# Performance work log

Measured on AMD Instinct MI355X. Metric: run time of the kernel, lower is better.

Reference implementation:

```python
import jax, jax.numpy as jnp
import numpy as np

B, T, I, H = 256, 512, 64, 128


def setup_inputs() -> dict:
    key = jax.random.key(0)
    ks = jax.random.split(key, 7)
    s_ih = 1.0 / np.sqrt(H)
    return {
        "inputs": jax.random.normal(ks[0], (B, T, I), dtype=jnp.float32),
        "h_prev": jax.random.normal(ks[1], (B, H), dtype=jnp.float32),
        "c_prev": jax.random.normal(ks[2], (B, H), dtype=jnp.float32),
        "W_ih": jax.random.uniform(ks[3], (4 * H, I), dtype=jnp.float32, minval=-s_ih, maxval=s_ih),
        "W_hh": jax.random.uniform(ks[4], (4 * H, H), dtype=jnp.float32, minval=-s_ih, maxval=s_ih),
        "b_ih": jax.random.uniform(ks[5], (4 * H,), dtype=jnp.float32, minval=-s_ih, maxval=s_ih),
        "b_hh": jax.random.uniform(ks[6], (4 * H,), dtype=jnp.float32, minval=-s_ih, maxval=s_ih),
    }


def reference(inputs, h_prev, c_prev, W_ih, W_hh, b_ih, b_hh):
    # Precompute input-to-gate projections for all timesteps in one GEMM: [B,T,4H]
    x_gates = jnp.einsum("bti,gi->btg", inputs, W_ih) + b_ih + b_hh

    def step(carry, xg):
        h, c = carry
        gates = xg + h @ W_hh.T  # [B, 4H]
        i_g, f_g, g_g, o_g = jnp.split(gates, 4, axis=-1)  # PyTorch i,f,g,o order
        i_g = jax.nn.sigmoid(i_g)
        f_g = jax.nn.sigmoid(f_g)
        g_g = jnp.tanh(g_g)
        o_g = jax.nn.sigmoid(o_g)
        c_next = f_g * c + i_g * g_g
        h_next = o_g * jnp.tanh(c_next)
        return (h_next, c_next), h_next

    (h_last, c_last), hs = jax.lax.scan(step, (h_prev, c_prev), jnp.swapaxes(x_gates, 0, 1))
    outputs = jnp.swapaxes(hs, 0, 1)  # [B, T, H]
    return outputs, h_last, c_last
```

## Files before the change

### kernel.cpp

```cpp
#include <hip/hip_runtime.h>


#define BB 256
#define TT 512
#define II 64
#define HH 128
#define KK 192
#define KS 8
#define KPT (KK / KS)
#define NTH (HH * KS)

static_assert(KPT % 4 == 0, "float4 granularity");

__device__ __forceinline__ float dpp_xor1(float v) {
    return __int_as_float(__builtin_amdgcn_mov_dpp(__float_as_int(v), 0xB1, 0xF, 0xF, true));
}
__device__ __forceinline__ float dpp_xor2(float v) {
    return __int_as_float(__builtin_amdgcn_mov_dpp(__float_as_int(v), 0x4E, 0xF, 0xF, true));
}
__device__ __forceinline__ float swz_xor4(float v) {
    return __int_as_float(__builtin_amdgcn_ds_swizzle(__float_as_int(v), 0x101F));
}
__device__ __forceinline__ float fast_sigmoid(float x) {
    float e = __expf(-x);
    return __builtin_amdgcn_rcpf(1.0f + e);
}
__device__ __forceinline__ float fast_tanh(float x) {
    float e = __expf(2.0f * x);
    return 1.0f - 2.0f * __builtin_amdgcn_rcpf(e + 1.0f);
}

__global__ __launch_bounds__(NTH, 4)
void lstm_split(const float* __restrict__ inputs,
                const float* __restrict__ h_prev,
                const float* __restrict__ c_prev,
                const float* __restrict__ W_ih,
                const float* __restrict__ W_hh,
                const float* __restrict__ b_ih,
                const float* __restrict__ b_hh,
                float* __restrict__ out)
{
    const int b   = blockIdx.x;
    const int tid = threadIdx.x;
    const int j   = tid >> 3;
    const int ks  = tid & 7;
    const int k0  = ks * KPT;

    float w[4][KPT];
    #pragma unroll
    for (int r = 0; r < 4; ++r) {
        const int row = j + r * HH;
        #pragma unroll
        for (int g = 0; g < KPT / 4; ++g) {
            const int k = k0 + 4 * g;
            float4 v = (k < II) ? *(const float4*)(W_ih + (size_t)row * II + k)
                                : *(const float4*)(W_hh + (size_t)row * HH + (k - II));
            w[r][4*g+0] = v.x; w[r][4*g+1] = v.y; w[r][4*g+2] = v.z; w[r][4*g+3] = v.w;
        }
    }
    float bias[4];
    #pragma unroll
    for (int r = 0; r < 4; ++r) {
        const int row = j + r * HH;
        bias[r] = (ks == 0) ? (b_ih[row] + b_hh[row]) : 0.0f;
    }

    __shared__ __align__(16) float xh[2][KK];

    float c = c_prev[(size_t)b * HH + j];
    float h = 0.0f;

    const float* xin = inputs + (size_t)b * TT * II;
    if (ks == 0) xh[0][II + j] = h_prev[(size_t)b * HH + j];
    if (tid < II) xh[0][tid] = xin[tid];
    __syncthreads();

    float* outp = out + (size_t)b * TT * HH;
    float* cur = xh[0];
    float* nxt = xh[1];

    for (int t = 0; t < TT; ++t) {
        float xpre = 0.0f;
        if (tid < II) {
            const int tn = (t + 1 < TT) ? (t + 1) : (TT - 1);
            xpre = xin[(size_t)tn * II + tid];
        }

        float a0 = bias[0], a1 = bias[1], a2 = bias[2], a3 = bias[3];
        const float4* xc = (const float4*)(cur + k0);
        #pragma unroll
        for (int g = 0; g < KPT / 4; ++g) {
            const float4 v = xc[g];
            a0 = fmaf(w[0][4*g+0], v.x, a0); a1 = fmaf(w[1][4*g+0], v.x, a1);
            a2 = fmaf(w[2][4*g+0], v.x, a2); a3 = fmaf(w[3][4*g+0], v.x, a3);
            a0 = fmaf(w[0][4*g+1], v.y, a0); a1 = fmaf(w[1][4*g+1], v.y, a1);
            a2 = fmaf(w[2][4*g+1], v.y, a2); a3 = fmaf(w[3][4*g+1], v.y, a3);
            a0 = fmaf(w[0][4*g+2], v.z, a0); a1 = fmaf(w[1][4*g+2], v.z, a1);
            a2 = fmaf(w[2][4*g+2], v.z, a2); a3 = fmaf(w[3][4*g+2], v.z, a3);
            a0 = fmaf(w[0][4*g+3], v.w, a0); a1 = fmaf(w[1][4*g+3], v.w, a1);
            a2 = fmaf(w[2][4*g+3], v.w, a2); a3 = fmaf(w[3][4*g+3], v.w, a3);
        }

        a0 += dpp_xor1(a0); a0 += dpp_xor2(a0); a0 += swz_xor4(a0);
        a1 += dpp_xor1(a1); a1 += dpp_xor2(a1); a1 += swz_xor4(a1);
        a2 += dpp_xor1(a2); a2 += dpp_xor2(a2); a2 += swz_xor4(a2);
        a3 += dpp_xor1(a3); a3 += dpp_xor2(a3); a3 += swz_xor4(a3);

        const float ig = fast_sigmoid(a0);
        const float fg = fast_sigmoid(a1);
        const float gg = fast_tanh(a2);
        const float og = fast_sigmoid(a3);
        c = fmaf(fg, c, ig * gg);
        h = og * fast_tanh(c);

        if (ks == 0) {
            nxt[II + j] = h;
            outp[(size_t)t * HH + j] = h;
        }
        if (tid < II) nxt[tid] = xpre;
        __syncthreads();
        float* tmp = cur; cur = nxt; nxt = tmp;
    }

    if (ks == 0) {
        out[(size_t)BB * TT * HH + (size_t)b * HH + j] = h;
        out[(size_t)BB * TT * HH + (size_t)BB * HH + (size_t)b * HH + j] = c;
    }
}

extern "C" void kernel_launch(void* const* d_in, const int* in_sizes, int n_in,
                              void* d_out, int out_size, void* d_ws, size_t ws_size,
                              hipStream_t stream) {
    const float* inputs = (const float*)d_in[0];
    const float* h_prev = (const float*)d_in[1];
    const float* c_prev = (const float*)d_in[2];
    const float* W_ih   = (const float*)d_in[3];
    const float* W_hh   = (const float*)d_in[4];
    const float* b_ih   = (const float*)d_in[5];
    const float* b_hh   = (const float*)d_in[6];
    float* outp = (float*)d_out;

    lstm_split<<<dim3(BB), dim3(NTH), 0, stream>>>(
        inputs, h_prev, c_prev, W_ih, W_hh, b_ih, b_hh, outp);
}
```

Measured before the change: 547.3 us.

## Split gates across lanes with 2-way K split and unified activation

Each thread now handles one gate row over half of the concatenated input/hidden vector (96 elements) instead of all four gates over one eighth. The per-step reduction drops to a single DPP add, and gate values are exchanged between lanes with DPP and swizzle. Tanh is expressed as a scaled sigmoid, so each lane computes one activation uniformly. This shortens the reduction and activation chain on the serial critical path. The cost is longer per-thread FMA chains (96 sequential FMAs into one accumulator) and extra cross-lane shuffles.

```diff
diff --git a/kernel.cpp b/kernel.cpp
--- a/kernel.cpp
+++ b/kernel.cpp
@@ -6,11 +6,8 @@
 #define II 64
 #define HH 128
 #define KK 192
-#define KS 8
-#define KPT (KK / KS)
-#define NTH (HH * KS)
-
-static_assert(KPT % 4 == 0, "float4 granularity");
+#define KPT 96
+#define NTH 1024
 
 __device__ __forceinline__ float dpp_xor1(float v) {
     return __int_as_float(__builtin_amdgcn_mov_dpp(__float_as_int(v), 0xB1, 0xF, 0xF, true));
@@ -21,49 +18,38 @@
 __device__ __forceinline__ float swz_xor4(float v) {
     return __int_as_float(__builtin_amdgcn_ds_swizzle(__float_as_int(v), 0x101F));
 }
-__device__ __forceinline__ float fast_sigmoid(float x) {
-    float e = __expf(-x);
-    return __builtin_amdgcn_rcpf(1.0f + e);
-}
-__device__ __forceinline__ float fast_tanh(float x) {
-    float e = __expf(2.0f * x);
-    return 1.0f - 2.0f * __builtin_amdgcn_rcpf(e + 1.0f);
-}
+__device__ __forceinline__ float fast_rcp(float x) { return __builtin_amdgcn_rcpf(x); }
 
-__global__ __launch_bounds__(NTH, 4)
-void lstm_split(const float* __restrict__ inputs,
-                const float* __restrict__ h_prev,
-                const float* __restrict__ c_prev,
-                const float* __restrict__ W_ih,
-                const float* __restrict__ W_hh,
-                const float* __restrict__ b_ih,
-                const float* __restrict__ b_hh,
-                float* __restrict__ out)
+__global__ __launch_bounds__(NTH)
+__attribute__((amdgpu_waves_per_eu(4, 4)))
+void lstm_gatesplit(const float* __restrict__ inputs,
+                    const float* __restrict__ h_prev,
+                    const float* __restrict__ c_prev,
+                    const float* __restrict__ W_ih,
+                    const float* __restrict__ W_hh,
+                    const float* __restrict__ b_ih,
+                    const float* __restrict__ b_hh,
+                    float* __restrict__ out)
 {
     const int b   = blockIdx.x;
     const int tid = threadIdx.x;
+    const int kh  = tid & 1;
+    const int r   = (tid >> 1) & 3;
     const int j   = tid >> 3;
-    const int ks  = tid & 7;
-    const int k0  = ks * KPT;
+    const int row = r * HH + j;
+    const int k0  = kh * KPT;
 
-    float w[4][KPT];
+    float w[KPT];
     #pragma unroll
-    for (int r = 0; r < 4; ++r) {
-        const int row = j + r * HH;
-        #pragma unroll
-        for (int g = 0; g < KPT / 4; ++g) {
-            const int k = k0 + 4 * g;
-            float4 v = (k < II) ? *(const float4*)(W_ih + (size_t)row * II + k)
-                                : *(const float4*)(W_hh + (size_t)row * HH + (k - II));
-            w[r][4*g+0] = v.x; w[r][4*g+1] = v.y; w[r][4*g+2] = v.z; w[r][4*g+3] = v.w;
-        }
+    for (int q = 0; q < KPT / 4; ++q) {
+        const int k = k0 + 4 * q;
+        float4 v = (k < II) ? *(const float4*)(W_ih + (size_t)row * II + k)
+                            : *(const float4*)(W_hh + (size_t)row * HH + (k - II));
+        w[4*q+0] = v.x; w[4*q+1] = v.y; w[4*q+2] = v.z; w[4*q+3] = v.w;
     }
-    float bias[4];
-    #pragma unroll
-    for (int r = 0; r < 4; ++r) {
-        const int row = j + r * HH;
-        bias[r] = (ks == 0) ? (b_ih[row] + b_hh[row]) : 0.0f;
-    }
+    const float bias = (kh == 0) ? (b_ih[row] + b_hh[row]) : 0.0f;
+    const float am = (r == 2) ? 2.0f : 1.0f;
+    const float ab = (r == 2) ? -1.0f : 0.0f;
 
     __shared__ __align__(16) float xh[2][KK];
 
@@ -71,8 +57,8 @@
     float h = 0.0f;
 
     const float* xin = inputs + (size_t)b * TT * II;
-    if (ks == 0) xh[0][II + j] = h_prev[(size_t)b * HH + j];
     if (tid < II) xh[0][tid] = xin[tid];
+    if ((tid & 7) == 0) xh[0][II + j] = h_prev[(size_t)b * HH + j];
     __syncthreads();
 
     float* outp = out + (size_t)b * TT * HH;
@@ -86,34 +72,32 @@
             xpre = xin[(size_t)tn * II + tid];
         }
 
-        float a0 = bias[0], a1 = bias[1], a2 = bias[2], a3 = bias[3];
+        float acc = bias;
         const float4* xc = (const float4*)(cur + k0);
         #pragma unroll
-        for (int g = 0; g < KPT / 4; ++g) {
-            const float4 v = xc[g];
-            a0 = fmaf(w[0][4*g+0], v.x, a0); a1 = fmaf(w[1][4*g+0], v.x, a1);
-            a2 = fmaf(w[2][4*g+0], v.x, a2); a3 = fmaf(w[3][4*g+0], v.x, a3);
-            a0 = fmaf(w[0][4*g+1], v.y, a0); a1 = fmaf(w[1][4*g+1], v.y, a1);
-            a2 = fmaf(w[2][4*g+1], v.y, a2); a3 = fmaf(w[3][4*g+1], v.y, a3);
-            a0 = fmaf(w[0][4*g+2], v.z, a0); a1 = fmaf(w[1][4*g+2], v.z, a1);
-            a2 = fmaf(w[2][4*g+2], v.z, a2); a3 = fmaf(w[3][4*g+2], v.z, a3);
-            a0 = fmaf(w[0][4*g+3], v.w, a0); a1 = fmaf(w[1][4*g+3], v.w, a1);
-            a2 = fmaf(w[2][4*g+3], v.w, a2); a3 = fmaf(w[3][4*g+3], v.w, a3);
+        for (int q = 0; q < KPT / 4; ++q) {
+            const float4 v = xc[q];
+            acc = fmaf(w[4*q+0], v.x, acc);
+            acc = fmaf(w[4*q+1], v.y, acc);
+            acc = fmaf(w[4*q+2], v.z, acc);
+            acc = fmaf(w[4*q+3], v.w, acc);
         }
 
-        a0 += dpp_xor1(a0); a0 += dpp_xor2(a0); a0 += swz_xor4(a0);
-        a1 += dpp_xor1(a1); a1 += dpp_xor2(a1); a1 += swz_xor4(a1);
-        a2 += dpp_xor1(a2); a2 += dpp_xor2(a2); a2 += swz_xor4(a2);
-        a3 += dpp_xor1(a3); a3 += dpp_xor2(a3); a3 += swz_xor4(a3);
+        acc += dpp_xor1(acc);
 
-        const float ig = fast_sigmoid(a0);
-        const float fg = fast_sigmoid(a1);
-        const float gg = fast_tanh(a2);
-        const float og = fast_sigmoid(a3);
-        c = fmaf(fg, c, ig * gg);
-        h = og * fast_tanh(c);
+        const float e = __expf(-(am * acc));
+        const float s = fast_rcp(1.0f + e);
+        const float a = fmaf(am, s, ab);
 
-        if (ks == 0) {
+        const float ig = a * swz_xor4(a);
+        const float f  = dpp_xor2(a);
+        const float o  = swz_xor4(f);
+        c = fmaf(f, c, ig);
+        const float e2 = __expf(-2.0f * c);
+        const float th = fmaf(2.0f, fast_rcp(1.0f + e2), -1.0f);
+        h = o * th;
+
+        if ((tid & 7) == 0) {
             nxt[II + j] = h;
             outp[(size_t)t * HH + j] = h;
         }
@@ -122,7 +106,7 @@
         float* tmp = cur; cur = nxt; nxt = tmp;
     }
 
-    if (ks == 0) {
+    if ((tid & 7) == 0) {
         out[(size_t)BB * TT * HH + (size_t)b * HH + j] = h;
         out[(size_t)BB * TT * HH + (size_t)BB * HH + (size_t)b * HH + j] = c;
     }
@@ -140,6 +124,6 @@
     const float* b_hh   = (const float*)d_in[6];
     float* outp = (float*)d_out;
 
-    lstm_split<<<dim3(BB), dim3(NTH), 0, stream>>>(
+    lstm_gatesplit<<<dim3(BB), dim3(NTH), 0, stream>>>(
         inputs, h_prev, c_prev, W_ih, W_hh, b_ih, b_hh, outp);
 }
```

New measurement: 604.2 us. +10.4%, slower.
